# Performance work log

Hardware: AMD Instinct MI355X
Metric: run time of the kernel (lower is better)

## Reference

```python
import jax, jax.numpy as jnp
import numpy as np

B, S, D = 8, 4096, 1024
G, V = 2, 320
TAU = 1.0
EPS = 1e-7


def setup_inputs() -> dict:
    key = jax.random.key(0)
    k_x, k_w, k_cb, k_u = jax.random.split(key, 4)
    x = jax.random.normal(k_x, (B, S, D), dtype=jnp.float32)
    W = jax.random.normal(k_w, (D, G * V), dtype=jnp.float32) * (1.0 / np.sqrt(D))
    b = jnp.zeros((G * V,), dtype=jnp.float32)
    # nn.init.uniform_ -> U(0,1); codebooks viewed as [G, V, D//G]
    codebooks = jax.random.uniform(k_cb, (G, V, D // G), dtype=jnp.float32)
    # standard Gumbel(0,1) noise, one per logit: shape [B*S*G, V]
    u = jax.random.uniform(k_u, (B * S * G, V), dtype=jnp.float32,
                           minval=1e-6, maxval=1.0 - 1e-6)
    gumbel = -jnp.log(-jnp.log(u))
    return {"x": x, "W": W, "b": b, "codebooks": codebooks, "gumbel": gumbel}


def reference(x, W, b, codebooks, gumbel):
    Bx, Sx, Dx = x.shape
    Gx, Vx, _ = codebooks.shape
    N = Bx * Sx
    # logit projection: [B,S,D] @ [D, G*V] -> flatten to [N*G, V]
    logits = (jnp.einsum('bsd,de->bse', x, W) + b).reshape(N * Gx, Vx)
    # gumbel-softmax, hard=True with straight-through estimator
    y_soft = jax.nn.softmax((logits + gumbel) / TAU, axis=-1)
    idx = jnp.argmax(y_soft, axis=-1)
    y_hard = jax.nn.one_hot(idx, Vx, dtype=y_soft.dtype)
    one_hot_st = y_hard + y_soft - jax.lax.stop_gradient(y_soft)  # fwd == y_hard
    # codebook lookup via (mostly one-hot) contraction: [N,G,V] x [G,V,d] -> [N,G,d]
    q = jnp.einsum('ngv,gvd->ngd', one_hot_st.reshape(N, Gx, Vx), codebooks)
    quantized = q.reshape(Bx, Sx, Dx)
    # perplexity from clean (non-gumbel) softmax probs
    probs = jax.nn.softmax(logits.reshape(N, Gx, Vx), axis=-1)
    avg_probs = probs.mean(axis=0)  # [G, V]
    perplexity = jnp.exp(-jnp.sum(avg_probs * jnp.log(avg_probs + EPS), axis=-1)).mean()
    return (quantized, perplexity)
```

## Files before the change

### kernel.cpp

```cpp
#include <hip/hip_runtime.h>
#include <hip/hip_bf16.h>
#include <math.h>

#define NROWS 32768
#define DD    1024
#define EE    640
#define VV    320
#define BM    128
#define KT    32
#define CTN   40

typedef __attribute__((ext_vector_type(8))) short short8;
typedef __attribute__((ext_vector_type(4))) short short4v;
typedef __attribute__((ext_vector_type(4))) float float4v;

static __device__ __forceinline__ unsigned short f2bf(float f) {
    unsigned int u = __float_as_uint(f);
    return (unsigned short)((u + 0x7fffu + ((u >> 16) & 1u)) >> 16);
}

static __device__ __forceinline__ void gload_lds16(const void* g, void* l) {
    __builtin_amdgcn_global_load_lds(
        (const __attribute__((address_space(1))) unsigned int*)g,
        (__attribute__((address_space(3))) unsigned int*)l, 16, 0, 0);
}

__global__ void pack_w(const float* __restrict__ W, unsigned short* __restrict__ bp)
{
    const int t = threadIdx.x;
    const int tile = blockIdx.x * 4 + (t >> 6);
    const int lane = t & 63;
    const int kt = tile / CTN, ct = tile % CTN;
    const int k0 = kt * 32 + (lane >> 4) * 8;
    const int col = ct * 16 + (lane & 15);
    unsigned short v1[8];
    #pragma unroll
    for (int e = 0; e < 8; ++e)
        v1[e] = f2bf(W[(size_t)(k0 + e) * EE + col]);
    *(short8*)(bp + ((size_t)tile * 64 + lane) * 8) = *(const short8*)v1;
}

__global__ __launch_bounds__(1024, 4) void logits_kernel(
    const float* __restrict__ x, const unsigned short* __restrict__ bp,
    const float* __restrict__ bias, const float* __restrict__ gum,
    int* __restrict__ gfidx, float* __restrict__ probs_acc)
{
    __shared__ unsigned short Bs[3][32 * EE];
    __shared__ unsigned short As[2][BM * 32];
    __shared__ float probs_blk[EE];
    __shared__ float pmax[8][BM];
    __shared__ float psum[8][BM];
    __shared__ int   pidx[8][BM];
    __shared__ float finv[BM][2];

    const int t    = threadIdx.x;
    const int lane = t & 63;
    const int w    = t >> 6;
    const int rg   = w >> 3;
    const int cg   = w & 7;
    const int n0   = blockIdx.x * BM;

    float4v acc[4][5];
    #pragma unroll
    for (int rf = 0; rf < 4; ++rf)
        #pragma unroll
        for (int ct = 0; ct < 5; ++ct)
            acc[rf][ct] = (float4v)0.f;

    const int r0 = t >> 3, kq0 = t & 7;
    const int abase = (r0 >> 4)*512 + ((r0 & 15) + ((kq0 >> 1) << 4))*8 + ((kq0 & 1) << 2);
    const float* xr = x + (size_t)(n0 + r0) * DD + kq0 * 4;

    auto writeA = [&](int bb, float4 v) {
        short4v s1;
        s1[0] = (short)f2bf(v.x); s1[1] = (short)f2bf(v.y);
        s1[2] = (short)f2bf(v.z); s1[3] = (short)f2bf(v.w);
        *(short4v*)&As[bb][abase] = s1;
    };
    const int q0 = t, q1 = t + 1024, q2 = (t < 512) ? t + 2048 : t + 1536;
    auto stageB = [&](int bb, int kt) {
        const unsigned short* src = bp + (size_t)kt * (32 * EE);
        gload_lds16(src + (size_t)q0 * 8, &Bs[bb][q0 * 8]);
        gload_lds16(src + (size_t)q1 * 8, &Bs[bb][q1 * 8]);
        gload_lds16(src + (size_t)q2 * 8, &Bs[bb][q2 * 8]);
    };

    auto kbody = [&](int i, int b0, int bstg, float4& curA, float4& nxtA) {
        asm volatile("s_waitcnt vmcnt(4) lgkmcnt(0)" ::: "memory");
        __builtin_amdgcn_s_barrier();
        __builtin_amdgcn_sched_barrier(0);
        if (i + 2 < KT) {
            stageB(bstg, i + 2);
            nxtA = *(const float4*)(xr + (size_t)(i + 2) * 32);
        }
        __builtin_amdgcn_sched_barrier(0);
        short8 af[4];
        #pragma unroll
        for (int rf = 0; rf < 4; ++rf)
            af[rf] = *(const short8*)&As[i & 1][(rg*4 + rf)*512 + lane*8];
        #pragma unroll
        for (int ct = 0; ct < 5; ++ct) {
            short8 bf = *(const short8*)&Bs[b0][((cg*5 + ct)*64 + lane)*8];
            #pragma unroll
            for (int rf = 0; rf < 4; ++rf)
                acc[rf][ct] = __builtin_amdgcn_mfma_f32_16x16x32_bf16(af[rf], bf, acc[rf][ct], 0, 0, 0);
        }
        __builtin_amdgcn_sched_barrier(0);
        if (i + 1 < KT) writeA((i + 1) & 1, curA);
    };

    float4 pA0, pA1;
    {
        stageB(0, 0);
        float4 a00 = *(const float4*)(xr);
        stageB(1, 1);
        pA0 = *(const float4*)(xr + 32);
        __builtin_amdgcn_sched_barrier(0);
        writeA(0, a00);
    }

    int bc = 0;
    for (int i = 0; i < KT; i += 2) {
        const int b1 = (bc + 1 > 2) ? 0 : bc + 1;
        const int b2 = (bc + 2 > 2) ? bc - 1 : bc + 2;
        kbody(i,     bc, b2, pA0, pA1);
        kbody(i + 1, b1, bc, pA1, pA0);
        bc = b2;
    }

    {
        float bv[5];
        #pragma unroll
        for (int ct = 0; ct < 5; ++ct) bv[ct] = bias[cg*80 + ct*16 + (lane & 15)];
        #pragma unroll
        for (int rf = 0; rf < 4; ++rf)
            #pragma unroll
            for (int ct = 0; ct < 5; ++ct) {
                acc[rf][ct][0] += bv[ct]; acc[rf][ct][1] += bv[ct];
                acc[rf][ct][2] += bv[ct]; acc[rf][ct][3] += bv[ct];
            }
    }

    const int g = cg >> 2;
    const int goff0 = (cg & 3)*80 + (lane & 15);
    #pragma unroll
    for (int rf = 0; rf < 4; ++rf) {
        #pragma unroll
        for (int r = 0; r < 4; ++r) {
            const int rowA = rg*64 + rf*16 + ((lane >> 4) << 2) + r;
            const float* grow = gum + ((size_t)(n0 + rowA)*2 + g)*VV + goff0;
            float m1 = -1e30f; int bi = 0; float es = 0.f;
            #pragma unroll
            for (int ct = 0; ct < 5; ++ct) {
                float z  = acc[rf][ct][r];
                float zg = z + grow[ct*16];
                if (zg > m1) { m1 = zg; bi = goff0 + ct*16; }
                es += __expf(z);
            }
            #pragma unroll
            for (int off = 1; off < 16; off <<= 1) {
                float om = __shfl_xor(m1, off);
                int   ob = __shfl_xor(bi, off);
                if (om > m1 || (om == m1 && ob < bi)) { m1 = om; bi = ob; }
                es += __shfl_xor(es, off);
            }
            if ((lane & 15) == 0) {
                pmax[cg][rowA] = m1; pidx[cg][rowA] = bi; psum[cg][rowA] = es;
            }
        }
    }
    for (int c = t; c < EE; c += 1024) probs_blk[c] = 0.f;
    __syncthreads();

    if (t < 256) {
        const int row = t & 127, gg = t >> 7;
        float m1 = -1e30f; int bi = 0x7fffffff; float s = 0.f;
        #pragma unroll
        for (int c = 0; c < 4; ++c) {
            const float om = pmax[gg*4 + c][row];
            const int   ob = pidx[gg*4 + c][row];
            if (om > m1 || (om == m1 && ob < bi)) { m1 = om; bi = ob; }
            s += psum[gg*4 + c][row];
        }
        gfidx[(size_t)(n0 + row)*2 + gg] = bi;
        finv[row][gg] = 1.f / s;
    }
    __syncthreads();

    float pacc[5];
    #pragma unroll
    for (int ct = 0; ct < 5; ++ct) pacc[ct] = 0.f;
    #pragma unroll
    for (int rf = 0; rf < 4; ++rf) {
        #pragma unroll
        for (int r = 0; r < 4; ++r) {
            const int rowA = rg*64 + rf*16 + ((lane >> 4) << 2) + r;
            const float inv = finv[rowA][g];
            #pragma unroll
            for (int ct = 0; ct < 5; ++ct)
                pacc[ct] += __expf(acc[rf][ct][r]) * inv;
        }
    }
    #pragma unroll
    for (int off = 16; off < 64; off <<= 1)
        #pragma unroll
        for (int ct = 0; ct < 5; ++ct)
            pacc[ct] += __shfl_xor(pacc[ct], off);
    if (lane < 16) {
        #pragma unroll
        for (int ct = 0; ct < 5; ++ct)
            atomicAdd(&probs_blk[cg*80 + ct*16 + lane], pacc[ct]);
    }
    __syncthreads();

    for (int c = t; c < EE; c += 1024)
        atomicAdd(&probs_acc[c], probs_blk[c]);
}

__global__ __launch_bounds__(256) void gather_kernel(
    const float* __restrict__ cb, const int* __restrict__ gfidx,
    const float* __restrict__ probs_acc, float* __restrict__ out, int out_size)
{
    __shared__ int sidx[8][2];
    __shared__ float s0[4], s1[4];
    const int t  = threadIdx.x;
    const int r0 = blockIdx.x * 8;
    if (t < 16) sidx[t >> 1][t & 1] = gfidx[(size_t)(r0 + (t >> 1)) * 2 + (t & 1)];
    __syncthreads();
    const int gg = t >> 7;
    const int f4 = t & 127;
    #pragma unroll
    for (int r = 0; r < 8; ++r) {
        const int idx = sidx[r][gg];
        const float4 v = *(const float4*)&cb[((size_t)gg*VV + idx)*512 + (size_t)f4*4];
        *(float4*)&out[(size_t)(r0 + r)*DD + (size_t)t*4] = v;
    }
    if (blockIdx.x == 0) {
        float p0 = 0.f, p1 = 0.f;
        for (int c = t; c < EE; c += 256) {
            float a = probs_acc[c] * (1.0f / NROWS);
            float v = a * logf(a + 1e-7f);
            if (c < VV) p0 += v; else p1 += v;
        }
        #pragma unroll
        for (int off = 1; off < 64; off <<= 1) {
            p0 += __shfl_xor(p0, off);
            p1 += __shfl_xor(p1, off);
        }
        if ((t & 63) == 0) { s0[t >> 6] = p0; s1[t >> 6] = p1; }
        __syncthreads();
        if (t == 0) {
            float a0 = s0[0] + s0[1] + s0[2] + s0[3];
            float a1 = s1[0] + s1[1] + s1[2] + s1[3];
            out[out_size - 1] = 0.5f * (expf(-a0) + expf(-a1));
        }
    }
}

extern "C" void kernel_launch(void* const* d_in, const int* in_sizes, int n_in,
                              void* d_out, int out_size, void* d_ws, size_t ws_size,
                              hipStream_t stream)
{
    const float* x   = (const float*)d_in[0];
    const float* W   = (const float*)d_in[1];
    const float* b   = (const float*)d_in[2];
    const float* cb  = (const float*)d_in[3];
    const float* gum = (const float*)d_in[4];
    float* out = (float*)d_out;

    unsigned short* bp = (unsigned short*)d_ws;
    float* probs_acc = (float*)((char*)d_ws + (size_t)DD*EE*2);
    int*   gfidx     = (int*)((char*)d_ws + (size_t)DD*EE*2 + 4096);

    hipMemsetAsync(probs_acc, 0, EE * sizeof(float), stream);
    pack_w<<<320, 256, 0, stream>>>(W, bp);
    logits_kernel<<<NROWS / BM, 1024, 0, stream>>>(x, bp, b, gum, gfidx, probs_acc);
    gather_kernel<<<NROWS / 8, 256, 0, stream>>>(cb, gfidx, probs_acc, out, out_size);
}
```

Before: 128.6 us.

## Split GEMM epilogue into separate kernel via bf16 logits buffer

Splits the fused GEMM-plus-epilogue into two kernels. A pure GEMM writes bias-added bf16 logits to workspace, and a separate epilogue kernel does the gumbel argmax, softmax probabilities and codebook gather, accumulating probabilities into 8 replicated global buffers. A small final kernel reduces the replicas and computes perplexity. The aim is to lighten the register and LDS load of the GEMM kernel and cut atomic contention, at the cost of an extra round trip of roughly 42MB of logits through memory, bf16 rounding of logits before the argmax, and more kernel launches.

New measurement: 204.5 us. 59.0% more time.

```diff
diff --git a/kernel.cpp b/kernel.cpp
--- a/kernel.cpp
+++ b/kernel.cpp
@@ -40,6 +40,174 @@
     *(short8*)(bp + ((size_t)tile * 64 + lane) * 8) = *(const short8*)v1;
 }
 
+__global__ __launch_bounds__(1024, 4) void gemm_z_kernel(
+    const float* __restrict__ x, const unsigned short* __restrict__ bp,
+    const float* __restrict__ bias, unsigned short* __restrict__ z)
+{
+    __shared__ unsigned short Bs[3][32 * EE];
+    __shared__ unsigned short As[2][BM * 32];
+
+    const int t    = threadIdx.x;
+    const int lane = t & 63;
+    const int w    = t >> 6;
+    const int rg   = w >> 3;
+    const int cg   = w & 7;
+    const int n0   = blockIdx.x * BM;
+
+    float4v acc[4][5];
+    #pragma unroll
+    for (int rf = 0; rf < 4; ++rf)
+        #pragma unroll
+        for (int ct = 0; ct < 5; ++ct)
+            acc[rf][ct] = (float4v)0.f;
+
+    const int r0 = t >> 3, kq0 = t & 7;
+    const int abase = (r0 >> 4)*512 + ((r0 & 15) + ((kq0 >> 1) << 4))*8 + ((kq0 & 1) << 2);
+    const float* xr = x + (size_t)(n0 + r0) * DD + kq0 * 4;
+
+    auto writeA = [&](int bb, float4 v) {
+        short4v s1;
+        s1[0] = (short)f2bf(v.x); s1[1] = (short)f2bf(v.y);
+        s1[2] = (short)f2bf(v.z); s1[3] = (short)f2bf(v.w);
+        *(short4v*)&As[bb][abase] = s1;
+    };
+    const int q0 = t, q1 = t + 1024, q2 = (t < 512) ? t + 2048 : t + 1536;
+    auto stageB = [&](int bb, int kt) {
+        const unsigned short* src = bp + (size_t)kt * (32 * EE);
+        gload_lds16(src + (size_t)q0 * 8, &Bs[bb][q0 * 8]);
+        gload_lds16(src + (size_t)q1 * 8, &Bs[bb][q1 * 8]);
+        gload_lds16(src + (size_t)q2 * 8, &Bs[bb][q2 * 8]);
+    };
+
+    auto kbody = [&](int i, int b0, int bstg, float4& curA, float4& nxtA) {
+        asm volatile("s_waitcnt vmcnt(4) lgkmcnt(0)" ::: "memory");
+        __builtin_amdgcn_s_barrier();
+        __builtin_amdgcn_sched_barrier(0);
+        if (i + 2 < KT) {
+            stageB(bstg, i + 2);
+            nxtA = *(const float4*)(xr + (size_t)(i + 2) * 32);
+        }
+        __builtin_amdgcn_sched_barrier(0);
+        short8 af[4];
+        #pragma unroll
+        for (int rf = 0; rf < 4; ++rf)
+            af[rf] = *(const short8*)&As[i & 1][(rg*4 + rf)*512 + lane*8];
+        #pragma unroll
+        for (int ct = 0; ct < 5; ++ct) {
+            short8 bf = *(const short8*)&Bs[b0][((cg*5 + ct)*64 + lane)*8];
+            #pragma unroll
+            for (int rf = 0; rf < 4; ++rf)
+                acc[rf][ct] = __builtin_amdgcn_mfma_f32_16x16x32_bf16(af[rf], bf, acc[rf][ct], 0, 0, 0);
+        }
+        __builtin_amdgcn_sched_barrier(0);
+        if (i + 1 < KT) writeA((i + 1) & 1, curA);
+    };
+
+    float4 pA0, pA1;
+    {
+        stageB(0, 0);
+        float4 a00 = *(const float4*)(xr);
+        stageB(1, 1);
+        pA0 = *(const float4*)(xr + 32);
+        __builtin_amdgcn_sched_barrier(0);
+        writeA(0, a00);
+    }
+
+    int bc = 0;
+    for (int i = 0; i < KT; i += 2) {
+        const int b1 = (bc + 1 > 2) ? 0 : bc + 1;
+        const int b2 = (bc + 2 > 2) ? bc - 1 : bc + 2;
+        kbody(i,     bc, b2, pA0, pA1);
+        kbody(i + 1, b1, bc, pA1, pA0);
+        bc = b2;
+    }
+
+    float bv[5];
+    const int cbase = (cg >> 2)*320 + (cg & 3)*80 + (lane & 15);
+    #pragma unroll
+    for (int ct = 0; ct < 5; ++ct) bv[ct] = bias[cbase + ct*16];
+    #pragma unroll
+    for (int rf = 0; rf < 4; ++rf) {
+        #pragma unroll
+        for (int r = 0; r < 4; ++r) {
+            const size_t n = (size_t)(n0 + rg*64 + rf*16 + ((lane >> 4) << 2) + r);
+            #pragma unroll
+            for (int ct = 0; ct < 5; ++ct)
+                z[n*EE + cbase + ct*16] = f2bf(acc[rf][ct][r] + bv[ct]);
+        }
+    }
+}
+
+__global__ __launch_bounds__(256, 4) void epi_kernel(
+    const unsigned short* __restrict__ z, const float* __restrict__ gum,
+    const float* __restrict__ cb, float* __restrict__ out,
+    float* __restrict__ probs_rep)
+{
+    __shared__ float probs_blk[EE];
+    __shared__ int   sidx[16][2];
+
+    const int t   = threadIdx.x;
+    const int row = t >> 4;
+    const int cgi = t & 15;
+    const size_t n = (size_t)blockIdx.x * 16 + row;
+    const int g = cgi >> 3;
+    const int vbase = (cgi & 7) * 40;
+
+    for (int c = t; c < EE; c += 256) probs_blk[c] = 0.f;
+
+    uint4 zp[5];
+    const uint4* zsrc = (const uint4*)(z + n*EE + cgi*40);
+    #pragma unroll
+    for (int i = 0; i < 5; ++i) zp[i] = zsrc[i];
+    float gv[40];
+    const float4* gsrc = (const float4*)(gum + ((n << 1) + g)*VV + vbase);
+    #pragma unroll
+    for (int i = 0; i < 10; ++i) {
+        float4 v = gsrc[i];
+        gv[4*i] = v.x; gv[4*i+1] = v.y; gv[4*i+2] = v.z; gv[4*i+3] = v.w;
+    }
+
+    float m1 = -1e30f; int bi = 0; float es = 0.f;
+    #pragma unroll
+    for (int j = 0; j < 40; ++j) {
+        const unsigned int u = ((const unsigned int*)zp)[j >> 1];
+        const float zj = __uint_as_float((j & 1) ? (u & 0xffff0000u) : (u << 16));
+        const float zg = zj + gv[j];
+        if (zg > m1) { m1 = zg; bi = vbase + j; }
+        es += __expf(zj);
+    }
+    #pragma unroll
+    for (int off = 1; off < 8; off <<= 1) {
+        float om = __shfl_xor(m1, off);
+        int   ob = __shfl_xor(bi, off);
+        if (om > m1 || (om == m1 && ob < bi)) { m1 = om; bi = ob; }
+        es += __shfl_xor(es, off);
+    }
+    const float inv = 1.f / es;
+    if ((cgi & 7) == 0) sidx[row][g] = bi;
+    __syncthreads();
+
+    #pragma unroll
+    for (int j = 0; j < 40; ++j) {
+        const unsigned int u = ((const unsigned int*)zp)[j >> 1];
+        const float zj = __uint_as_float((j & 1) ? (u & 0xffff0000u) : (u << 16));
+        atomicAdd(&probs_blk[g*VV + vbase + j], __expf(zj) * inv);
+    }
+
+    #pragma unroll 4
+    for (int k = 0; k < 16; ++k) {
+        const int gg  = t >> 7;
+        const int idx = sidx[k][gg];
+        const float4 v = *(const float4*)&cb[((size_t)gg*VV + idx)*512 + (size_t)(t & 127)*4];
+        *(float4*)&out[((size_t)blockIdx.x*16 + k)*DD + (size_t)t*4] = v;
+    }
+    __syncthreads();
+
+    const int rep = blockIdx.x & 7;
+    for (int c = t; c < EE; c += 256)
+        atomicAdd(&probs_rep[rep*EE + c], probs_blk[c]);
+}
+
 __global__ __launch_bounds__(1024, 4) void logits_kernel(
     const float* __restrict__ x, const unsigned short* __restrict__ bp,
     const float* __restrict__ bias, const float* __restrict__ gum,
@@ -84,7 +252,6 @@
         gload_lds16(src + (size_t)q1 * 8, &Bs[bb][q1 * 8]);
         gload_lds16(src + (size_t)q2 * 8, &Bs[bb][q2 * 8]);
     };
-
     auto kbody = [&](int i, int b0, int bstg, float4& curA, float4& nxtA) {
         asm volatile("s_waitcnt vmcnt(4) lgkmcnt(0)" ::: "memory");
         __builtin_amdgcn_s_barrier();
@@ -118,7 +285,6 @@
         __builtin_amdgcn_sched_barrier(0);
         writeA(0, a00);
     }
-
     int bc = 0;
     for (int i = 0; i < KT; i += 2) {
         const int b1 = (bc + 1 > 2) ? 0 : bc + 1;
@@ -152,10 +318,10 @@
             float m1 = -1e30f; int bi = 0; float es = 0.f;
             #pragma unroll
             for (int ct = 0; ct < 5; ++ct) {
-                float z  = acc[rf][ct][r];
-                float zg = z + grow[ct*16];
+                float zv  = acc[rf][ct][r];
+                float zg = zv + grow[ct*16];
                 if (zg > m1) { m1 = zg; bi = goff0 + ct*16; }
-                es += __expf(z);
+                es += __expf(zv);
             }
             #pragma unroll
             for (int off = 1; off < 16; off <<= 1) {
@@ -212,48 +378,53 @@
             atomicAdd(&probs_blk[cg*80 + ct*16 + lane], pacc[ct]);
     }
     __syncthreads();
-
     for (int c = t; c < EE; c += 1024)
         atomicAdd(&probs_acc[c], probs_blk[c]);
 }
 
 __global__ __launch_bounds__(256) void gather_kernel(
     const float* __restrict__ cb, const int* __restrict__ gfidx,
-    const float* __restrict__ probs_acc, float* __restrict__ out, int out_size)
+    float* __restrict__ out)
 {
     __shared__ int sidx[8][2];
-    __shared__ float s0[4], s1[4];
     const int t  = threadIdx.x;
     const int r0 = blockIdx.x * 8;
     if (t < 16) sidx[t >> 1][t & 1] = gfidx[(size_t)(r0 + (t >> 1)) * 2 + (t & 1)];
     __syncthreads();
     const int gg = t >> 7;
-    const int f4 = t & 127;
     #pragma unroll
     for (int r = 0; r < 8; ++r) {
         const int idx = sidx[r][gg];
-        const float4 v = *(const float4*)&cb[((size_t)gg*VV + idx)*512 + (size_t)f4*4];
+        const float4 v = *(const float4*)&cb[((size_t)gg*VV + idx)*512 + (size_t)(t & 127)*4];
         *(float4*)&out[(size_t)(r0 + r)*DD + (size_t)t*4] = v;
     }
-    if (blockIdx.x == 0) {
-        float p0 = 0.f, p1 = 0.f;
-        for (int c = t; c < EE; c += 256) {
-            float a = probs_acc[c] * (1.0f / NROWS);
-            float v = a * logf(a + 1e-7f);
-            if (c < VV) p0 += v; else p1 += v;
-        }
-        #pragma unroll
-        for (int off = 1; off < 64; off <<= 1) {
-            p0 += __shfl_xor(p0, off);
-            p1 += __shfl_xor(p1, off);
-        }
-        if ((t & 63) == 0) { s0[t >> 6] = p0; s1[t >> 6] = p1; }
-        __syncthreads();
-        if (t == 0) {
-            float a0 = s0[0] + s0[1] + s0[2] + s0[3];
-            float a1 = s1[0] + s1[1] + s1[2] + s1[3];
-            out[out_size - 1] = 0.5f * (expf(-a0) + expf(-a1));
-        }
+}
+
+__global__ void perp8_kernel(const float* __restrict__ probs_rep,
+                             float* __restrict__ outp)
+{
+    __shared__ float s0[4], s1[4];
+    int t = threadIdx.x;
+    float p0 = 0.f, p1 = 0.f;
+    for (int c = t; c < EE; c += 256) {
+        float a = 0.f;
+        #pragma unroll
+        for (int rp = 0; rp < 8; ++rp) a += probs_rep[rp*EE + c];
+        a *= (1.0f / NROWS);
+        float v = a * logf(a + 1e-7f);
+        if (c < VV) p0 += v; else p1 += v;
+    }
+    #pragma unroll
+    for (int off = 1; off < 64; off <<= 1) {
+        p0 += __shfl_xor(p0, off);
+        p1 += __shfl_xor(p1, off);
+    }
+    if ((t & 63) == 0) { s0[t >> 6] = p0; s1[t >> 6] = p1; }
+    __syncthreads();
+    if (t == 0) {
+        float a0 = s0[0] + s0[1] + s0[2] + s0[3];
+        float a1 = s1[0] + s1[1] + s1[2] + s1[3];
+        outp[0] = 0.5f * (expf(-a0) + expf(-a1));
     }
 }
 
@@ -268,12 +439,24 @@
     const float* gum = (const float*)d_in[4];
     float* out = (float*)d_out;
 
-    unsigned short* bp = (unsigned short*)d_ws;
-    float* probs_acc = (float*)((char*)d_ws + (size_t)DD*EE*2);
-    int*   gfidx     = (int*)((char*)d_ws + (size_t)DD*EE*2 + 4096);
-
-    hipMemsetAsync(probs_acc, 0, EE * sizeof(float), stream);
+    char* wsp = (char*)d_ws;
+    unsigned short* bp = (unsigned short*)wsp;
+    const size_t bp_b = (size_t)DD*EE*2;
+    float* probs_rep = (float*)(wsp + bp_b);
+    const size_t pr_b = 8*EE*sizeof(float);
+    int* gfidx = (int*)(wsp + bp_b + pr_b);
+    const size_t gi_b = (size_t)NROWS*2*sizeof(int);
+    unsigned short* z = (unsigned short*)(wsp + bp_b + pr_b + gi_b);
+    const size_t need = bp_b + pr_b + gi_b + (size_t)NROWS*EE*2;
+
+    hipMemsetAsync(probs_rep, 0, pr_b, stream);
     pack_w<<<320, 256, 0, stream>>>(W, bp);
-    logits_kernel<<<NROWS / BM, 1024, 0, stream>>>(x, bp, b, gum, gfidx, probs_acc);
-    gather_kernel<<<NROWS / 8, 256, 0, stream>>>(cb, gfidx, probs_acc, out, out_size);
-}
+    if (ws_size >= need) {
+        gemm_z_kernel<<<NROWS / BM, 1024, 0, stream>>>(x, bp, b, z);
+        epi_kernel<<<NROWS / 16, 256, 0, stream>>>(z, gum, cb, out, probs_rep);
+    } else {
+        logits_kernel<<<NROWS / BM, 1024, 0, stream>>>(x, bp, b, gum, gfidx, probs_rep);
+        gather_kernel<<<NROWS / 8, 256, 0, stream>>>(cb, gfidx, out);
+    }
+    perp8_kernel<<<1, 256, 0, stream>>>(probs_rep, out + (out_size - 1));
+}
```
